# Optimization experiments

Measured on AMD Instinct MI355X. Metric: run time of the kernel, lower is better.

Reference implementation:

```python
import jax, jax.numpy as jnp
import numpy as np

NQ = 4   # qubits
QL = 2   # strongly-entangling layers
Z_DIAG = jnp.array([1.0, -1.0], jnp.float32)


def _apply_1q_batched(state, U, w):
    # state: [B,2,2,2,2], U: [B,2,2] per-sample gate on wire w
    st = jnp.moveaxis(state, 1 + w, -1)
    st = jnp.einsum('b...i,bji->b...j', st, U)
    return jnp.moveaxis(st, -1, 1 + w)


def _apply_1q_shared(state, U, w):
    # U: [2,2] shared gate on wire w
    st = jnp.moveaxis(state, 1 + w, -1)
    st = jnp.einsum('b...i,ji->b...j', st, U)
    return jnp.moveaxis(st, -1, 1 + w)


def _cnot(state, c, t):
    c_ax, t_ax = 1 + c, 1 + t
    s0 = jax.lax.index_in_dim(state, 0, c_ax, keepdims=True)
    s1 = jax.lax.index_in_dim(state, 1, c_ax, keepdims=True)
    s1 = jnp.flip(s1, axis=t_ax)  # X on target where control==1
    return jnp.concatenate([s0, s1], axis=c_ax)


def _rot_matrix(phi, th, om):
    # PennyLane Rot = RZ(om) RY(th) RZ(phi)
    ct, st = jnp.cos(th * 0.5), jnp.sin(th * 0.5)
    return jnp.stack([
        jnp.stack([jnp.exp(-0.5j * (phi + om)) * ct, -jnp.exp(0.5j * (phi - om)) * st]),
        jnp.stack([jnp.exp(-0.5j * (phi - om)) * st, jnp.exp(0.5j * (phi + om)) * ct]),
    ])


def _quantum(angles, qw):
    # angles: [B,4] RX embedding angles; qw: [QL,NQ,3]
    B = angles.shape[0]
    state = jnp.zeros((B,) + (2,) * NQ, jnp.complex64)
    state = state.at[(slice(None),) + (0,) * NQ].set(1.0)
    # AngleEmbedding: RX(angle_w) on wire w (per-sample gates)
    half = angles.astype(jnp.float32) * 0.5
    c, s = jnp.cos(half), jnp.sin(half)
    for w in range(NQ):
        U = jnp.stack([
            jnp.stack([c[:, w] + 0j, -1j * s[:, w]], -1),
            jnp.stack([-1j * s[:, w], c[:, w] + 0j], -1),
        ], -2)  # [B,2,2]
        state = _apply_1q_batched(state, U, w)
    # StronglyEntanglingLayers: Rot on each wire, then CNOT ring with range r
    qwc = qw.astype(jnp.complex64).real  # keep real, cast inside rot
    for l in range(QL):
        for w in range(NQ):
            U = _rot_matrix(qw[l, w, 0], qw[l, w, 1], qw[l, w, 2])
            state = _apply_1q_shared(state, U, w)
        r = l % (NQ - 1) + 1  # default ranges: [1, 2]
        for w in range(NQ):
            state = _cnot(state, w, (w + r) % NQ)
    probs = state.real ** 2 + state.imag ** 2  # [B,2,2,2,2]
    evs = []
    for w in range(NQ):
        other = tuple(a for a in range(1, NQ + 1) if a != 1 + w)
        evs.append(probs.sum(axis=other) @ Z_DIAG)  # <Z_w>
    return jnp.stack(evs, -1)  # [B,NQ]


def _lstm_last(x, W_ih, W_hh, b_ih, b_hh):
    # torch gate order: i, f, g, o; returns last hidden state [B,H]
    B = x.shape[0]
    H = W_hh.shape[1]
    xz = jnp.einsum('btf,gf->btg', x, W_ih) + b_ih + b_hh  # [B,T,4H]
    def step(carry, z_t):
        h, c = carry
        z = z_t + h @ W_hh.T
        i, f, g, o = jnp.split(z, 4, axis=-1)
        i, f, o = jax.nn.sigmoid(i), jax.nn.sigmoid(f), jax.nn.sigmoid(o)
        g = jnp.tanh(g)
        c = f * c + i * g
        h = o * jnp.tanh(c)
        return (h, c), None
    h0 = jnp.zeros((B, H), x.dtype)
    (h, _), _ = jax.lax.scan(step, (h0, h0), jnp.swapaxes(xz, 0, 1))
    return h


def setup_inputs() -> dict:
    key = jax.random.key(0)
    ks = jax.random.split(key, 10)
    B, T, IN, H = 4096, 256, 1, 50
    sc_ih = 1.0 / np.sqrt(H)
    return {
        'x': jax.random.normal(ks[0], (B, T, IN), jnp.float32),
        'W_ih': jax.random.normal(ks[1], (4 * H, IN), jnp.float32) * sc_ih,
        'W_hh': jax.random.normal(ks[2], (4 * H, H), jnp.float32) * sc_ih,
        'b_ih': jax.random.normal(ks[3], (4 * H,), jnp.float32) * sc_ih,
        'b_hh': jax.random.normal(ks[4], (4 * H,), jnp.float32) * sc_ih,
        'Wp': jax.random.normal(ks[5], (NQ, H), jnp.float32) * sc_ih,
        'bp': jax.random.normal(ks[6], (NQ,), jnp.float32) * sc_ih,
        'qw': jax.random.uniform(ks[7], (QL, NQ, 3), jnp.float32, 0.0, 2.0 * np.pi),
        'Wo': jax.random.normal(ks[8], (1, NQ), jnp.float32) * 0.5,
        'bo': jax.random.normal(ks[9], (1,), jnp.float32) * 0.5,
    }


def reference(x, W_ih, W_hh, b_ih, b_hh, Wp, bp, qw, Wo, bo):
    h = _lstm_last(x, W_ih, W_hh, b_ih, b_hh)          # [B,H]
    angles = jnp.tanh(h @ Wp.T + bp) * (np.pi / 2)     # [B,NQ]
    evs = _quantum(angles, qw)                          # [B,NQ]
    return evs @ Wo.T + bo                              # [B,1]
```

## Files before the change

kernel.cpp:

```cpp
#include <hip/hip_runtime.h>

#define HID 50
#define TSTEPS 256
#define SPB 16
#define NW 13
#define THREADS (NW * 64)
#define XSTRIDE 257

#if __has_builtin(__builtin_amdgcn_exp2f)
#define EXP2(x) __builtin_amdgcn_exp2f(x)
#else
#define EXP2(x) exp2f(x)
#endif
#define L2E 1.44269504088896340736f

typedef __attribute__((ext_vector_type(8))) _Float16 half8;
typedef __attribute__((ext_vector_type(4))) float f32x4;

static __device__ __forceinline__ f32x4 MF16(half8 a, half8 b, f32x4 c) {
    return __builtin_amdgcn_mfma_f32_16x16x32_f16(a, b, c, 0, 0, 0);
}
static __device__ __forceinline__ float sig2(float a) {
    return __builtin_amdgcn_rcpf(1.0f + EXP2(a));
}
static __device__ __forceinline__ float fast_tanh(float x) {
    return 1.0f - 2.0f * sig2(2.0f * L2E * x);
}

static __device__ __forceinline__ int slot_of_unit(int u) {
    return 8 * (u >> 3) + 2 * (u & 3) + ((u >> 2) & 1);
}

__global__ __launch_bounds__(THREADS, 4) void hybrid_lstm_fp16(
    const float* __restrict__ x,
    const float* __restrict__ W_ih,
    const float* __restrict__ W_hh,
    const float* __restrict__ b_ih,
    const float* __restrict__ b_hh,
    const float* __restrict__ Wp,
    const float* __restrict__ bp,
    const float* __restrict__ qw,
    const float* __restrict__ Wo,
    const float* __restrict__ bo,
    float* __restrict__ out)
{
    __shared__ __align__(16) float x_lds[SPB * XSTRIDE];
    __shared__ __align__(16) _Float16 h_tab[2][1024];

    const int tid  = threadIdx.x;
    const int wid  = tid >> 6;
    const int lane = tid & 63;
    const int qs   = lane & 15;
    const int g2   = lane >> 4;

    {
        unsigned* hz = (unsigned*)&h_tab[0][0];
        for (int i = tid; i < 1024; i += THREADS) hz[i] = 0u;
        const float* xg = x + (size_t)blockIdx.x * SPB * TSTEPS;
        for (int i = tid; i < SPB * TSTEPS; i += THREADS)
            x_lds[(i >> 8) * XSTRIDE + (i & 255)] = xg[i];
    }

    half8 Ah[2];
    {
        const int uA   = 4 * wid + (qs >> 2);
        const bool vr  = (uA < HID);
        const int q    = qs & 3;
        const float sc = (q == 2) ? 2.0f * L2E : -L2E;
        const int orow = q * HID + (vr ? uA : 0);
#pragma unroll
        for (int kh = 0; kh < 2; ++kh) {
#pragma unroll
            for (int r = 0; r < 8; ++r) {
                const int s  = kh * 32 + g2 * 8 + r;
                const int ws = 2 * (s >> 3) + (s & 1);
                const int un = 4 * ws + ((s >> 1) & 3);
                float v = 0.0f;
                if (vr && un < HID) v = sc * W_hh[orow * HID + un];
                Ah[kh][r] = (_Float16)v;
            }
        }
    }

    const int u   = 4 * wid + g2;
    const bool uv = (u < HID);
    float wih4[4], bsum4[4];
#pragma unroll
    for (int reg = 0; reg < 4; ++reg) {
        const float sc = (reg == 2) ? 2.0f * L2E : -L2E;
        const int orow = reg * HID + (uv ? u : 0);
        wih4[reg]  = sc * W_ih[orow];
        bsum4[reg] = sc * (b_ih[orow] + b_hh[orow]);
    }

    const int s_w = slot_of_unit(uv ? u : 0);
    const int p_w = s_w & 31;
    _Float16* const wp0 = &h_tab[0][(s_w >> 5) * 512 + ((p_w >> 3) * 16 + qs) * 8 + (p_w & 7)];

    __syncthreads();

    float cst = 0.0f;
    half8 bh0, bh1;

    auto loadB = [&](int buf) {
        const _Float16* bp_ = &h_tab[buf][0] + lane * 8;
        bh0 = *(const half8*)(bp_);
        bh1 = *(const half8*)(bp_ + 512);
    };

    loadB(1);
    float xt = x_lds[qs * XSTRIDE];

#pragma unroll 2
    for (int t = 0; t < TSTEPS; ++t) {
        f32x4 acc;
#pragma unroll
        for (int reg = 0; reg < 4; ++reg)
            acc[reg] = fmaf(wih4[reg], xt, bsum4[reg]);
        acc = MF16(Ah[0], bh0, acc);
        acc = MF16(Ah[1], bh1, acc);

        const float ig = sig2(acc[0]);
        const float fg = sig2(acc[1]);
        const float gg = 1.0f - 2.0f * sig2(acc[2]);
        const float og = sig2(acc[3]);
        cst = fmaf(fg, cst, ig * gg);
        const float h = og * fast_tanh(cst);

        const float xn = x_lds[qs * XSTRIDE + t + 1];
        if (uv) wp0[(t & 1) * 1024] = (_Float16)h;
        __syncthreads();
        loadB(t & 1);
        xt = xn;
    }

    if (wid < 8 && lane < 32) {
        const int sm  = 2 * wid + (lane >> 4);
        const int ql  = lane & 15;
        const int grp = lane & 48;

        const _Float16* t1 = &h_tab[1][0];
        float ang0 = bp[0], ang1 = bp[1], ang2 = bp[2], ang3 = bp[3];
#pragma unroll
        for (int k = 0; k < HID; ++k) {
            const int s   = slot_of_unit(k);
            const int p   = s & 31;
            const int idx = (s >> 5) * 512 + ((p >> 3) * 16 + sm) * 8 + (p & 7);
            const float hk = (float)t1[idx];
            ang0 = fmaf(Wp[0 * HID + k], hk, ang0);
            ang1 = fmaf(Wp[1 * HID + k], hk, ang1);
            ang2 = fmaf(Wp[2 * HID + k], hk, ang2);
            ang3 = fmaf(Wp[3 * HID + k], hk, ang3);
        }
        float ang[4];
        ang[0] = fast_tanh(ang0) * 1.57079632679489662f;
        ang[1] = fast_tanh(ang1) * 1.57079632679489662f;
        ang[2] = fast_tanh(ang2) * 1.57079632679489662f;
        ang[3] = fast_tanh(ang3) * 1.57079632679489662f;

        float ar = (ql == 0) ? 1.0f : 0.0f;
        float ai = 0.0f;

#pragma unroll
        for (int wq = 0; wq < 4; ++wq) {
            const int mask = 8 >> wq;
            float s_, c_;
            __sincosf(0.5f * ang[wq], &s_, &c_);
            const float pr = __shfl_xor(ar, mask);
            const float pi = __shfl_xor(ai, mask);
            const float nr = c_ * ar + s_ * pi;
            const float ni = c_ * ai - s_ * pr;
            ar = nr; ai = ni;
        }
#pragma unroll
        for (int l = 0; l < 2; ++l) {
#pragma unroll
            for (int wq = 0; wq < 4; ++wq) {
                const float phi = qw[(l * 4 + wq) * 3 + 0];
                const float th  = qw[(l * 4 + wq) * 3 + 1];
                const float om  = qw[(l * 4 + wq) * 3 + 2];
                float st_, ct_, sa, ca, sb, cb;
                __sincosf(0.5f * th, &st_, &ct_);
                __sincosf(0.5f * (phi + om), &sa, &ca);
                __sincosf(0.5f * (phi - om), &sb, &cb);
                const int mask = 8 >> wq;
                const bool bit = (ql & mask) != 0;
                const float dr  = ca * ct_;
                const float di  = (bit ? sa : -sa) * ct_;
                const float orr = (bit ? cb : -cb) * st_;
                const float oi  = -sb * st_;
                const float pr = __shfl_xor(ar, mask);
                const float pi = __shfl_xor(ai, mask);
                const float nr = dr * ar - di * ai + orr * pr - oi * pi;
                const float ni = dr * ai + di * ar + orr * pi + oi * pr;
                ar = nr; ai = ni;
            }
            const int r = (l % 3) + 1;
#pragma unroll
            for (int wq = 0; wq < 4; ++wq) {
                const int mc  = 8 >> wq;
                const int mt  = 8 >> ((wq + r) % 4);
                const int src = (ql & mc) ? (ql ^ mt) : ql;
                ar = __shfl(ar, grp | src);
                ai = __shfl(ai, grp | src);
            }
        }
        const float prob = ar * ar + ai * ai;
        float coeff = 0.0f;
#pragma unroll
        for (int wq = 0; wq < 4; ++wq) {
            const float sgn = (ql & (8 >> wq)) ? -1.0f : 1.0f;
            coeff = fmaf(sgn, Wo[wq], coeff);
        }
        float v = prob * coeff;
        v += __shfl_xor(v, 1);
        v += __shfl_xor(v, 2);
        v += __shfl_xor(v, 4);
        v += __shfl_xor(v, 8);
        if (ql == 0) out[blockIdx.x * SPB + sm] = v + bo[0];
    }
}

extern "C" void kernel_launch(void* const* d_in, const int* in_sizes, int n_in,
                              void* d_out, int out_size, void* d_ws, size_t ws_size,
                              hipStream_t stream) {
    const float* x    = (const float*)d_in[0];
    const float* W_ih = (const float*)d_in[1];
    const float* W_hh = (const float*)d_in[2];
    const float* b_ih = (const float*)d_in[3];
    const float* b_hh = (const float*)d_in[4];
    const float* Wp   = (const float*)d_in[5];
    const float* bp   = (const float*)d_in[6];
    const float* qw   = (const float*)d_in[7];
    const float* Wo   = (const float*)d_in[8];
    const float* bo   = (const float*)d_in[9];
    float* out = (float*)d_out;

    const int B = in_sizes[0] / TSTEPS;
    hybrid_lstm_fp16<<<B / SPB, THREADS, 0, stream>>>(x, W_ih, W_hh, b_ih, b_hh,
                                                      Wp, bp, qw, Wo, bo, out);
}
```

Baseline: 109.1 us.

## Halve samples per block and give each wave two unit tiles with lane shuffles

Cuts samples per block from 16 to 8 and waves from 13 to 7, so each wave now computes two 4-unit MFMA tiles (8 units) per step. The MFMA output columns are 8 samples duplicated, and results from the second tile are moved across with xor-8 shuffles so every lane handles one unit-sample pair. The h table layout is simplified to a unit-contiguous row per sample. The goal is twice as many blocks with smaller per-step barriers, which should give better occupancy and shorter sync latency on the serial recurrence. The cost is two extra MFMAs and four shuffles per step, and half of each MFMA's columns are wasted.

```diff
diff --git a/kernel.cpp b/kernel.cpp
--- a/kernel.cpp
+++ b/kernel.cpp
@@ -2,8 +2,8 @@
 
 #define HID 50
 #define TSTEPS 256
-#define SPB 16
-#define NW 13
+#define SPB 8
+#define NW 7
 #define THREADS (NW * 64)
 #define XSTRIDE 257
 
@@ -27,11 +27,7 @@
     return 1.0f - 2.0f * sig2(2.0f * L2E * x);
 }
 
-static __device__ __forceinline__ int slot_of_unit(int u) {
-    return 8 * (u >> 3) + 2 * (u & 3) + ((u >> 2) & 1);
-}
-
-__global__ __launch_bounds__(THREADS, 4) void hybrid_lstm_fp16(
+__global__ __launch_bounds__(THREADS, 4) void hybrid_lstm_fp16b(
     const float* __restrict__ x,
     const float* __restrict__ W_ih,
     const float* __restrict__ W_hh,
@@ -61,80 +57,98 @@
             x_lds[(i >> 8) * XSTRIDE + (i & 255)] = xg[i];
     }
 
-    half8 Ah[2];
+    half8 Ah[2][2];
     {
-        const int uA   = 4 * wid + (qs >> 2);
-        const bool vr  = (uA < HID);
         const int q    = qs & 3;
         const float sc = (q == 2) ? 2.0f * L2E : -L2E;
-        const int orow = q * HID + (vr ? uA : 0);
-#pragma unroll
-        for (int kh = 0; kh < 2; ++kh) {
-#pragma unroll
-            for (int r = 0; r < 8; ++r) {
-                const int s  = kh * 32 + g2 * 8 + r;
-                const int ws = 2 * (s >> 3) + (s & 1);
-                const int un = 4 * ws + ((s >> 1) & 3);
-                float v = 0.0f;
-                if (vr && un < HID) v = sc * W_hh[orow * HID + un];
-                Ah[kh][r] = (_Float16)v;
+#pragma unroll
+        for (int ti = 0; ti < 2; ++ti) {
+            const int uA  = 8 * wid + 4 * ti + (qs >> 2);
+            const bool vr = (uA < HID);
+            const int orow = q * HID + (vr ? uA : 0);
+#pragma unroll
+            for (int kh = 0; kh < 2; ++kh) {
+#pragma unroll
+                for (int r = 0; r < 8; ++r) {
+                    const int un = kh * 32 + g2 * 8 + r;
+                    float v = 0.0f;
+                    if (vr && un < HID) v = sc * W_hh[orow * HID + un];
+                    Ah[ti][kh][r] = (_Float16)v;
+                }
             }
         }
     }
 
-    const int u   = 4 * wid + g2;
-    const bool uv = (u < HID);
-    float wih4[4], bsum4[4];
-#pragma unroll
-    for (int reg = 0; reg < 4; ++reg) {
-        const float sc = (reg == 2) ? 2.0f * L2E : -L2E;
-        const int orow = reg * HID + (uv ? u : 0);
-        wih4[reg]  = sc * W_ih[orow];
-        bsum4[reg] = sc * (b_ih[orow] + b_hh[orow]);
-    }
-
-    const int s_w = slot_of_unit(uv ? u : 0);
-    const int p_w = s_w & 31;
-    _Float16* const wp0 = &h_tab[0][(s_w >> 5) * 512 + ((p_w >> 3) * 16 + qs) * 8 + (p_w & 7)];
+    float wihc[2][4], bsumc[2][4];
+#pragma unroll
+    for (int ti = 0; ti < 2; ++ti) {
+        const int uC  = 8 * wid + 4 * ti + g2;
+        const bool cv = (uC < HID);
+#pragma unroll
+        for (int reg = 0; reg < 4; ++reg) {
+            const float sc = (reg == 2) ? 2.0f * L2E : -L2E;
+            const int orow = reg * HID + (cv ? uC : 0);
+            wihc[ti][reg]  = sc * W_ih[orow];
+            bsumc[ti][reg] = sc * (b_ih[orow] + b_hh[orow]);
+        }
+    }
+
+    const int s_l = qs & 7;
+    const int u_l = 8 * wid + 4 * (qs >> 3) + g2;
+    const bool wv = (u_l < HID);
+    _Float16* const wp0 = &h_tab[0][(u_l >> 5) * 512 + s_l * 32 + (u_l & 31)];
 
     __syncthreads();
 
     float cst = 0.0f;
     half8 bh0, bh1;
-
     auto loadB = [&](int buf) {
-        const _Float16* bp_ = &h_tab[buf][0] + lane * 8;
+        const _Float16* bp_ = &h_tab[buf][qs * 32 + g2 * 8];
         bh0 = *(const half8*)(bp_);
         bh1 = *(const half8*)(bp_ + 512);
     };
 
     loadB(1);
-    float xt = x_lds[qs * XSTRIDE];
+    float xt = x_lds[s_l * XSTRIDE];
+    const bool hi8 = (qs >= 8);
 
 #pragma unroll 2
     for (int t = 0; t < TSTEPS; ++t) {
-        f32x4 acc;
-#pragma unroll
-        for (int reg = 0; reg < 4; ++reg)
-            acc[reg] = fmaf(wih4[reg], xt, bsum4[reg]);
-        acc = MF16(Ah[0], bh0, acc);
-        acc = MF16(Ah[1], bh1, acc);
-
-        const float ig = sig2(acc[0]);
-        const float fg = sig2(acc[1]);
-        const float gg = 1.0f - 2.0f * sig2(acc[2]);
-        const float og = sig2(acc[3]);
+        f32x4 acc0, acc1;
+#pragma unroll
+        for (int reg = 0; reg < 4; ++reg) {
+            acc0[reg] = fmaf(wihc[0][reg], xt, bsumc[0][reg]);
+            acc1[reg] = fmaf(wihc[1][reg], xt, bsumc[1][reg]);
+        }
+        acc0 = MF16(Ah[0][0], bh0, acc0);
+        acc1 = MF16(Ah[1][0], bh0, acc1);
+        acc0 = MF16(Ah[0][1], bh1, acc0);
+        acc1 = MF16(Ah[1][1], bh1, acc1);
+
+        const float r0 = __shfl_xor(acc1[0], 8);
+        const float r1 = __shfl_xor(acc1[1], 8);
+        const float r2 = __shfl_xor(acc1[2], 8);
+        const float r3 = __shfl_xor(acc1[3], 8);
+        const float a0 = hi8 ? r0 : acc0[0];
+        const float a1 = hi8 ? r1 : acc0[1];
+        const float a2 = hi8 ? r2 : acc0[2];
+        const float a3 = hi8 ? r3 : acc0[3];
+
+        const float ig = sig2(a0);
+        const float fg = sig2(a1);
+        const float gg = 1.0f - 2.0f * sig2(a2);
+        const float og = sig2(a3);
         cst = fmaf(fg, cst, ig * gg);
         const float h = og * fast_tanh(cst);
 
-        const float xn = x_lds[qs * XSTRIDE + t + 1];
-        if (uv) wp0[(t & 1) * 1024] = (_Float16)h;
+        const float xn = x_lds[s_l * XSTRIDE + t + 1];
+        if (wv) wp0[(t & 1) * 1024] = (_Float16)h;
         __syncthreads();
         loadB(t & 1);
         xt = xn;
     }
 
-    if (wid < 8 && lane < 32) {
+    if (wid < 4 && lane < 32) {
         const int sm  = 2 * wid + (lane >> 4);
         const int ql  = lane & 15;
         const int grp = lane & 48;
@@ -143,9 +157,7 @@
         float ang0 = bp[0], ang1 = bp[1], ang2 = bp[2], ang3 = bp[3];
 #pragma unroll
         for (int k = 0; k < HID; ++k) {
-            const int s   = slot_of_unit(k);
-            const int p   = s & 31;
-            const int idx = (s >> 5) * 512 + ((p >> 3) * 16 + sm) * 8 + (p & 7);
+            const int idx = (k >> 5) * 512 + sm * 32 + (k & 31);
             const float hk = (float)t1[idx];
             ang0 = fmaf(Wp[0 * HID + k], hk, ang0);
             ang1 = fmaf(Wp[1 * HID + k], hk, ang1);
@@ -237,6 +249,6 @@
     float* out = (float*)d_out;
 
     const int B = in_sizes[0] / TSTEPS;
-    hybrid_lstm_fp16<<<B / SPB, THREADS, 0, stream>>>(x, W_ih, W_hh, b_ih, b_hh,
-                                                      Wp, bp, qw, Wo, bo, out);
-}
+    hybrid_lstm_fp16b<<<B / SPB, THREADS, 0, stream>>>(x, W_ih, W_hh, b_ih, b_hh,
+                                                       Wp, bp, qw, Wo, bo, out);
+}
```

After: 136.9 us. 25.5% more time.

## Run each LSTM as a single wavefront with register-resident h and no block barriers

Applied to the files above, without the earlier changes.

Replaces the 13-wave block that shares h through LDS and synchronises every timestep with one 64-lane wavefront per 4 samples. All W_hh tiles stay in registers and h is redistributed with ds_bpermute, so no LDS traffic or __syncthreads is needed. The input and bias are folded into the MFMA K dimension, with x split into hi/lo fp16 halves. The cost is heavy register pressure from 13x2 half8 tiles, many more MFMAs per lane, and far more blocks of tiny size, so occupancy and spilling are the main risks.

```diff
diff --git a/kernel.cpp b/kernel.cpp
--- a/kernel.cpp
+++ b/kernel.cpp
@@ -2,20 +2,17 @@
 
 #define HID 50
 #define TSTEPS 256
-#define SPB 16
-#define NW 13
-#define THREADS (NW * 64)
-#define XSTRIDE 257
+#define L2E 1.44269504088896340736f
 
 #if __has_builtin(__builtin_amdgcn_exp2f)
 #define EXP2(x) __builtin_amdgcn_exp2f(x)
 #else
 #define EXP2(x) exp2f(x)
 #endif
-#define L2E 1.44269504088896340736f
 
 typedef __attribute__((ext_vector_type(8))) _Float16 half8;
 typedef __attribute__((ext_vector_type(4))) float f32x4;
+typedef __attribute__((ext_vector_type(4))) int int4v;
 
 static __device__ __forceinline__ f32x4 MF16(half8 a, half8 b, f32x4 c) {
     return __builtin_amdgcn_mfma_f32_16x16x32_f16(a, b, c, 0, 0, 0);
@@ -26,12 +23,15 @@
 static __device__ __forceinline__ float fast_tanh(float x) {
     return 1.0f - 2.0f * sig2(2.0f * L2E * x);
 }
-
-static __device__ __forceinline__ int slot_of_unit(int u) {
-    return 8 * (u >> 3) + 2 * (u & 3) + ((u >> 2) & 1);
-}
-
-__global__ __launch_bounds__(THREADS, 4) void hybrid_lstm_fp16(
+static __device__ __forceinline__ float bperm(int idx, float v) {
+    return __int_as_float(__builtin_amdgcn_ds_bpermute(idx, __float_as_int(v)));
+}
+static __device__ __forceinline__ unsigned h16(float v) {
+    _Float16 h = (_Float16)v;
+    return (unsigned)__builtin_bit_cast(unsigned short, h);
+}
+
+__global__ __launch_bounds__(64, 1) void hybrid_lstm_wl(
     const float* __restrict__ x,
     const float* __restrict__ W_ih,
     const float* __restrict__ W_hh,
@@ -44,181 +44,205 @@
     const float* __restrict__ bo,
     float* __restrict__ out)
 {
-    __shared__ __align__(16) float x_lds[SPB * XSTRIDE];
-    __shared__ __align__(16) _Float16 h_tab[2][1024];
-
-    const int tid  = threadIdx.x;
-    const int wid  = tid >> 6;
-    const int lane = tid & 63;
-    const int qs   = lane & 15;
-    const int g2   = lane >> 4;
-
+    const int lane = threadIdx.x & 63;
+    const int qs = lane & 15;
+    const int G  = lane >> 4;
+    const int s  = qs & 3;
+    const int o  = qs >> 2;
+
+    half8 Ah[13][2];
     {
-        unsigned* hz = (unsigned*)&h_tab[0][0];
-        for (int i = tid; i < 1024; i += THREADS) hz[i] = 0u;
-        const float* xg = x + (size_t)blockIdx.x * SPB * TSTEPS;
-        for (int i = tid; i < SPB * TSTEPS; i += THREADS)
-            x_lds[(i >> 8) * XSTRIDE + (i & 255)] = xg[i];
-    }
-
-    half8 Ah[2];
-    {
-        const int uA   = 4 * wid + (qs >> 2);
-        const bool vr  = (uA < HID);
-        const int q    = qs & 3;
-        const float sc = (q == 2) ? 2.0f * L2E : -L2E;
-        const int orow = q * HID + (vr ? uA : 0);
-#pragma unroll
-        for (int kh = 0; kh < 2; ++kh) {
-#pragma unroll
-            for (int r = 0; r < 8; ++r) {
-                const int s  = kh * 32 + g2 * 8 + r;
-                const int ws = 2 * (s >> 3) + (s & 1);
-                const int un = 4 * ws + ((s >> 1) & 3);
-                float v = 0.0f;
-                if (vr && un < HID) v = sc * W_hh[orow * HID + un];
-                Ah[kh][r] = (_Float16)v;
-            }
-        }
-    }
-
-    const int u   = 4 * wid + g2;
-    const bool uv = (u < HID);
-    float wih4[4], bsum4[4];
-#pragma unroll
-    for (int reg = 0; reg < 4; ++reg) {
-        const float sc = (reg == 2) ? 2.0f * L2E : -L2E;
-        const int orow = reg * HID + (uv ? u : 0);
-        wih4[reg]  = sc * W_ih[orow];
-        bsum4[reg] = sc * (b_ih[orow] + b_hh[orow]);
-    }
-
-    const int s_w = slot_of_unit(uv ? u : 0);
-    const int p_w = s_w & 31;
-    _Float16* const wp0 = &h_tab[0][(s_w >> 5) * 512 + ((p_w >> 3) * 16 + qs) * 8 + (p_w & 7)];
-
-    __syncthreads();
-
-    float cst = 0.0f;
-    half8 bh0, bh1;
-
-    auto loadB = [&](int buf) {
-        const _Float16* bp_ = &h_tab[buf][0] + lane * 8;
-        bh0 = *(const half8*)(bp_);
-        bh1 = *(const half8*)(bp_ + 512);
-    };
-
-    loadB(1);
-    float xt = x_lds[qs * XSTRIDE];
-
-#pragma unroll 2
-    for (int t = 0; t < TSTEPS; ++t) {
-        f32x4 acc;
-#pragma unroll
-        for (int reg = 0; reg < 4; ++reg)
-            acc[reg] = fmaf(wih4[reg], xt, bsum4[reg]);
-        acc = MF16(Ah[0], bh0, acc);
-        acc = MF16(Ah[1], bh1, acc);
-
-        const float ig = sig2(acc[0]);
-        const float fg = sig2(acc[1]);
-        const float gg = 1.0f - 2.0f * sig2(acc[2]);
-        const float og = sig2(acc[3]);
-        cst = fmaf(fg, cst, ig * gg);
-        const float h = og * fast_tanh(cst);
-
-        const float xn = x_lds[qs * XSTRIDE + t + 1];
-        if (uv) wp0[(t & 1) * 1024] = (_Float16)h;
-        __syncthreads();
-        loadB(t & 1);
-        xt = xn;
-    }
-
-    if (wid < 8 && lane < 32) {
-        const int sm  = 2 * wid + (lane >> 4);
-        const int ql  = lane & 15;
-        const int grp = lane & 48;
-
-        const _Float16* t1 = &h_tab[1][0];
-        float ang0 = bp[0], ang1 = bp[1], ang2 = bp[2], ang3 = bp[3];
-#pragma unroll
-        for (int k = 0; k < HID; ++k) {
-            const int s   = slot_of_unit(k);
-            const int p   = s & 31;
-            const int idx = (s >> 5) * 512 + ((p >> 3) * 16 + sm) * 8 + (p & 7);
-            const float hk = (float)t1[idx];
-            ang0 = fmaf(Wp[0 * HID + k], hk, ang0);
-            ang1 = fmaf(Wp[1 * HID + k], hk, ang1);
-            ang2 = fmaf(Wp[2 * HID + k], hk, ang2);
-            ang3 = fmaf(Wp[3 * HID + k], hk, ang3);
-        }
-        float ang[4];
-        ang[0] = fast_tanh(ang0) * 1.57079632679489662f;
-        ang[1] = fast_tanh(ang1) * 1.57079632679489662f;
-        ang[2] = fast_tanh(ang2) * 1.57079632679489662f;
-        ang[3] = fast_tanh(ang3) * 1.57079632679489662f;
-
-        float ar = (ql == 0) ? 1.0f : 0.0f;
-        float ai = 0.0f;
-
+        const int gate = qs & 3;
+        const float sc = (gate == 2) ? 2.0f * L2E : -L2E;
+#pragma unroll
+        for (int T = 0; T < 13; ++T) {
+            const int uA = 4 * T + o;
+            const bool vr = (uA < HID);
+            const int orow = gate * HID + (vr ? uA : 0);
+#pragma unroll
+            for (int c = 0; c < 2; ++c) {
+#pragma unroll
+                for (int r = 0; r < 8; ++r) {
+                    const int k = 32 * c + 8 * G + r;
+                    float v = 0.0f;
+                    if (vr) {
+                        if (k < HID)                 v = sc * W_hh[orow * HID + k];
+                        else if (k == 50 || k == 51) v = sc * W_ih[orow];
+                        else if (k == 52)            v = sc * (b_ih[orow] + b_hh[orow]);
+                    }
+                    Ah[T][c][r] = (_Float16)v;
+                }
+            }
+        }
+    }
+
+    int idxm[4];
+#pragma unroll
+    for (int m = 0; m < 4; ++m) idxm[m] = (16 * m + s + 4 * G) * 4;
+
+    const bool ob0 = (o & 1) != 0;
+    const bool ob1 = (o & 2) != 0;
+
+    float hreg[4] = {0.0f, 0.0f, 0.0f, 0.0f};
+    float cst[4]  = {0.0f, 0.0f, 0.0f, 0.0f};
+    const f32x4 zq = {0.0f, 0.0f, 0.0f, 0.0f};
+
+    const float* xg = x + (size_t)(blockIdx.x * 4 + s) * TSTEPS;
+    float4 xq = *(const float4*)xg;
+
+#pragma unroll 1
+    for (int t4 = 0; t4 < TSTEPS; t4 += 4) {
+        const int tn = (t4 + 4 < TSTEPS) ? (t4 + 4) : (TSTEPS - 4);
+        const float4 xqn = *(const float4*)(xg + tn);
+#pragma unroll
+        for (int kk = 0; kk < 4; ++kk) {
+            const float xt = (kk == 0) ? xq.x : (kk == 1) ? xq.y : (kk == 2) ? xq.z : xq.w;
+            const _Float16 xh = (_Float16)xt;
+            const unsigned xdw = h16(xt) | (h16(xt - (float)xh) << 16);
+
+            unsigned dw0[4], dw1[4];
+#pragma unroll
+            for (int d = 0; d < 4; ++d) {
+                const int e0 = 2 * d, e1 = 2 * d + 1;
+                const float a0 = bperm(idxm[e0 & 3], hreg[(e0 >> 2)]);
+                const float a1 = bperm(idxm[e1 & 3], hreg[(e1 >> 2)]);
+                dw0[d] = h16(a0) | (h16(a1) << 16);
+                const float b0 = bperm(idxm[e0 & 3], hreg[2 + (e0 >> 2)]);
+                const float b1 = bperm(idxm[e1 & 3], hreg[2 + (e1 >> 2)]);
+                dw1[d] = h16(b0) | (h16(b1) << 16);
+            }
+            dw1[1] = (G == 2) ? xdw : dw1[1];
+            dw1[2] = (G == 2) ? 0x00003C00u : dw1[2];
+            const int4v i0 = {(int)dw0[0], (int)dw0[1], (int)dw0[2], (int)dw0[3]};
+            const int4v i1 = {(int)dw1[0], (int)dw1[1], (int)dw1[2], (int)dw1[3]};
+            const half8 bh0 = __builtin_bit_cast(half8, i0);
+            const half8 bh1 = __builtin_bit_cast(half8, i1);
+
+            f32x4 acc[13];
+#pragma unroll
+            for (int T = 0; T < 13; ++T) acc[T] = MF16(Ah[T][0], bh0, zq);
+#pragma unroll
+            for (int T = 0; T < 13; ++T) acc[T] = MF16(Ah[T][1], bh1, acc[T]);
+
+            f32x4 cell[4];
+#pragma unroll
+            for (int r = 0; r < 4; ++r) {
+                const float a01 = ob0 ? acc[2][r]  : acc[0][r];
+                const float a23 = ob0 ? acc[6][r]  : acc[4][r];
+                cell[0][r] = ob1 ? a23 : a01;
+                const float b01 = ob0 ? acc[3][r]  : acc[1][r];
+                const float b23 = ob0 ? acc[7][r]  : acc[5][r];
+                cell[1][r] = ob1 ? b23 : b01;
+                const float c01 = ob0 ? acc[10][r] : acc[8][r];
+                const float c23 = ob0 ? acc[8][r]  : acc[12][r];
+                cell[2][r] = ob1 ? c23 : c01;
+                const float d01 = ob0 ? acc[11][r] : acc[9][r];
+                cell[3][r] = ob1 ? acc[9][r] : d01;
+            }
+
+#pragma unroll
+            for (int j = 0; j < 4; ++j) {
+                const float ig = sig2(cell[j][0]);
+                const float fg = sig2(cell[j][1]);
+                const float gg = 1.0f - 2.0f * sig2(cell[j][2]);
+                const float og = sig2(cell[j][3]);
+                cst[j] = fmaf(fg, cst[j], ig * gg);
+                hreg[j] = og * fast_tanh(cst[j]);
+            }
+        }
+        xq = xqn;
+    }
+
+    float ang[4];
+#pragma unroll
+    for (int q = 0; q < 4; ++q) ang[q] = (G == 0) ? bp[q] : 0.0f;
+#pragma unroll
+    for (int c = 0; c < 2; ++c) {
+#pragma unroll
+        for (int e = 0; e < 8; ++e) {
+            const int u = 32 * c + 8 * G + e;
+            const float hv = bperm(idxm[e & 3], hreg[2 * c + (e >> 2)]);
+#pragma unroll
+            for (int q = 0; q < 4; ++q) {
+                const float w = (u < HID) ? Wp[q * HID + u] : 0.0f;
+                ang[q] = fmaf(w, hv, ang[q]);
+            }
+        }
+    }
+#pragma unroll
+    for (int q = 0; q < 4; ++q) {
+        ang[q] += __shfl_xor(ang[q], 16);
+        ang[q] += __shfl_xor(ang[q], 32);
+    }
+    const int sm  = lane >> 4;
+    const int ql  = lane & 15;
+    const int grp = lane & 48;
+    const int idxg = sm * 4;
+    float angc[4];
+#pragma unroll
+    for (int q = 0; q < 4; ++q)
+        angc[q] = fast_tanh(bperm(idxg, ang[q])) * 1.57079632679489662f;
+
+    float ar = (ql == 0) ? 1.0f : 0.0f;
+    float ai = 0.0f;
+
+#pragma unroll
+    for (int wq = 0; wq < 4; ++wq) {
+        const int mask = 8 >> wq;
+        float s_, c_;
+        __sincosf(0.5f * angc[wq], &s_, &c_);
+        const float pr = __shfl_xor(ar, mask);
+        const float pi = __shfl_xor(ai, mask);
+        const float nr = c_ * ar + s_ * pi;
+        const float ni = c_ * ai - s_ * pr;
+        ar = nr; ai = ni;
+    }
+#pragma unroll
+    for (int l = 0; l < 2; ++l) {
 #pragma unroll
         for (int wq = 0; wq < 4; ++wq) {
+            const float phi = qw[(l * 4 + wq) * 3 + 0];
+            const float th  = qw[(l * 4 + wq) * 3 + 1];
+            const float om  = qw[(l * 4 + wq) * 3 + 2];
+            float st_, ct_, sa, ca, sb, cb;
+            __sincosf(0.5f * th, &st_, &ct_);
+            __sincosf(0.5f * (phi + om), &sa, &ca);
+            __sincosf(0.5f * (phi - om), &sb, &cb);
             const int mask = 8 >> wq;
-            float s_, c_;
-            __sincosf(0.5f * ang[wq], &s_, &c_);
+            const bool bit = (ql & mask) != 0;
+            const float dr  = ca * ct_;
+            const float di  = (bit ? sa : -sa) * ct_;
+            const float orr = (bit ? cb : -cb) * st_;
+            const float oi  = -sb * st_;
             const float pr = __shfl_xor(ar, mask);
             const float pi = __shfl_xor(ai, mask);
-            const float nr = c_ * ar + s_ * pi;
-            const float ni = c_ * ai - s_ * pr;
+            const float nr = dr * ar - di * ai + orr * pr - oi * pi;
+            const float ni = dr * ai + di * ar + orr * pi + oi * pr;
             ar = nr; ai = ni;
         }
-#pragma unroll
-        for (int l = 0; l < 2; ++l) {
-#pragma unroll
-            for (int wq = 0; wq < 4; ++wq) {
-                const float phi = qw[(l * 4 + wq) * 3 + 0];
-                const float th  = qw[(l * 4 + wq) * 3 + 1];
-                const float om  = qw[(l * 4 + wq) * 3 + 2];
-                float st_, ct_, sa, ca, sb, cb;
-                __sincosf(0.5f * th, &st_, &ct_);
-                __sincosf(0.5f * (phi + om), &sa, &ca);
-                __sincosf(0.5f * (phi - om), &sb, &cb);
-                const int mask = 8 >> wq;
-                const bool bit = (ql & mask) != 0;
-                const float dr  = ca * ct_;
-                const float di  = (bit ? sa : -sa) * ct_;
-                const float orr = (bit ? cb : -cb) * st_;
-                const float oi  = -sb * st_;
-                const float pr = __shfl_xor(ar, mask);
-                const float pi = __shfl_xor(ai, mask);
-                const float nr = dr * ar - di * ai + orr * pr - oi * pi;
-                const float ni = dr * ai + di * ar + orr * pi + oi * pr;
-                ar = nr; ai = ni;
-            }
-            const int r = (l % 3) + 1;
-#pragma unroll
-            for (int wq = 0; wq < 4; ++wq) {
-                const int mc  = 8 >> wq;
-                const int mt  = 8 >> ((wq + r) % 4);
-                const int src = (ql & mc) ? (ql ^ mt) : ql;
-                ar = __shfl(ar, grp | src);
-                ai = __shfl(ai, grp | src);
-            }
-        }
-        const float prob = ar * ar + ai * ai;
-        float coeff = 0.0f;
+        const int r = (l % 3) + 1;
 #pragma unroll
         for (int wq = 0; wq < 4; ++wq) {
-            const float sgn = (ql & (8 >> wq)) ? -1.0f : 1.0f;
-            coeff = fmaf(sgn, Wo[wq], coeff);
-        }
-        float v = prob * coeff;
-        v += __shfl_xor(v, 1);
-        v += __shfl_xor(v, 2);
-        v += __shfl_xor(v, 4);
-        v += __shfl_xor(v, 8);
-        if (ql == 0) out[blockIdx.x * SPB + sm] = v + bo[0];
-    }
+            const int mc  = 8 >> wq;
+            const int mt  = 8 >> ((wq + r) % 4);
+            const int src = (ql & mc) ? (ql ^ mt) : ql;
+            ar = __shfl(ar, grp | src);
+            ai = __shfl(ai, grp | src);
+        }
+    }
+    const float prob = ar * ar + ai * ai;
+    float coeff = 0.0f;
+#pragma unroll
+    for (int wq = 0; wq < 4; ++wq) {
+        const float sgn = (ql & (8 >> wq)) ? -1.0f : 1.0f;
+        coeff = fmaf(sgn, Wo[wq], coeff);
+    }
+    float v = prob * coeff;
+    v += __shfl_xor(v, 1);
+    v += __shfl_xor(v, 2);
+    v += __shfl_xor(v, 4);
+    v += __shfl_xor(v, 8);
+    if (ql == 0) out[blockIdx.x * 4 + sm] = v + bo[0];
 }
 
 extern "C" void kernel_launch(void* const* d_in, const int* in_sizes, int n_in,
@@ -237,6 +261,6 @@
     float* out = (float*)d_out;
 
     const int B = in_sizes[0] / TSTEPS;
-    hybrid_lstm_fp16<<<B / SPB, THREADS, 0, stream>>>(x, W_ih, W_hh, b_ih, b_hh,
-                                                      Wp, bp, qw, Wo, bo, out);
-}
+    hybrid_lstm_wl<<<B / 4, 64, 0, stream>>>(x, W_ih, W_hh, b_ih, b_hh,
+                                             Wp, bp, qw, Wo, bo, out);
+}
```

New measurement: 191.5 us. 75.6% more time.
